# Optimization experiments

Hardware: AMD Instinct MI355X
Metric: run time of the kernel (lower is better)

The kernel has to match this reference:

```python
import jax, jax.numpy as jnp
import numpy as np

B, S, D = 4, 512, 128


def setup_inputs() -> dict:
    key = jax.random.key(0)
    ks = jax.random.split(key, 9)
    scale = 1.0 / np.sqrt(D)
    return {
        "inputs": jax.random.normal(ks[0], (B, S, D), dtype=jnp.float32),
        "encoder_outputs": jax.random.normal(ks[1], (B, S, D), dtype=jnp.float32),
        "mask": jax.random.randint(ks[2], (B, S), 0, 2, dtype=jnp.int32),
        "W1": jax.random.uniform(ks[3], (D, D), jnp.float32, -scale, scale),
        "b1": jax.random.uniform(ks[4], (D,), jnp.float32, -scale, scale),
        "W2": jax.random.uniform(ks[5], (D, D), jnp.float32, -scale, scale),
        "b2": jax.random.uniform(ks[6], (D,), jnp.float32, -scale, scale),
        "v_w": jax.random.uniform(ks[7], (D,), jnp.float32, -scale, scale),
        "v_b": jax.random.uniform(ks[8], (1,), jnp.float32, -scale, scale),
    }


def reference(inputs, encoder_outputs, mask, W1, b1, W2, b2, v_w, v_b):
    # key_out: W1(encoder_outputs)  [B, S_k, D]
    key_out = jnp.einsum("bkd,de->bke", encoder_outputs, W1) + b1
    # query_out: W2(inputs)        [B, S_q, D]
    query_out = jnp.einsum("bqd,de->bqe", inputs, W2) + b2
    # additive attention, all query positions at once: [B, S_q, S_k, D]
    t = jnp.tanh(key_out[:, None, :, :] + query_out[:, :, None, :])
    ui = jnp.einsum("bqkd,d->bqk", t, v_w) + v_b[0]
    # mask out padded key positions for every query position
    valid = mask.astype(bool)[:, None, :]  # [B, 1, S_k]
    logits = jnp.where(valid, ui, -jnp.inf)
    preds = jnp.argmax(logits, axis=-1)
    return (logits, preds)
```

## Files before the change

kernel.cpp:

```cpp
#include <hip/hip_runtime.h>
#include <math.h>

#define NB 4
#define NS 512
#define ND 128

static constexpr float K2LE = 2.885390081777927f;

__device__ inline float fast_exp2(float x){
#if __has_builtin(__builtin_amdgcn_exp2f)
  return __builtin_amdgcn_exp2f(x);
#else
  float r; asm("v_exp_f32 %0, %1" : "=v"(r) : "v"(x)); return r;
#endif
}
__device__ inline float fast_rcp(float x){
#if __has_builtin(__builtin_amdgcn_rcpf)
  return __builtin_amdgcn_rcpf(x);
#else
  float r; asm("v_rcp_f32 %0, %1" : "=v"(r) : "v"(x)); return r;
#endif
}

__global__ __launch_bounds__(256) void proj_kernel(
    const float* __restrict__ inputs, const float* __restrict__ enc,
    const float* __restrict__ W1, const float* __restrict__ b1,
    const float* __restrict__ W2, const float* __restrict__ b2,
    const float* __restrict__ vw, const float* __restrict__ vb,
    float* __restrict__ EKT, float* __restrict__ RQ, float* __restrict__ WQ,
    float* __restrict__ Csum){
  const int ROWS = 16;
  int blk = blockIdx.x;
  int t = threadIdx.x;

  if (blk == 256){
    if (t < 64){
      float v = vw[t] + vw[t + 64];
      #pragma unroll
      for (int off = 32; off; off >>= 1) v += __shfl_down(v, off);
      if (t == 0) Csum[0] = v + vb[0];
    }
    return;
  }

  bool is_key = (blk < 128);
  int rbase = (is_key ? blk : blk - 128) * ROWS;
  const float* X    = is_key ? enc : inputs;
  const float* W    = is_key ? W1  : W2;
  const float* bias = is_key ? b1  : b2;

  __shared__ float rows[ROWS][ND];
  {
    const float4* src = (const float4*)(X + (size_t)rbase*ND);
    float4* dst = (float4*)(&rows[0][0]);
    dst[t]       = src[t];
    dst[t + 256] = src[t + 256];
  }
  __syncthreads();

  int rg = t >> 5;
  int ec = (t & 31) * 4;
  float4 b4 = *(const float4*)(bias + ec);
  float4 acc0 = b4, acc1 = b4;
  const float* r0 = rows[rg];
  const float* r1 = rows[rg + 8];
  const float* wp = W + ec;
  #pragma unroll 4
  for (int d = 0; d < ND; ++d){
    float4 w4 = *(const float4*)(wp + (size_t)d*ND);
    float a = r0[d], c = r1[d];
    acc0.x = fmaf(a, w4.x, acc0.x);  acc1.x = fmaf(c, w4.x, acc1.x);
    acc0.y = fmaf(a, w4.y, acc0.y);  acc1.y = fmaf(c, w4.y, acc1.y);
    acc0.z = fmaf(a, w4.z, acc0.z);  acc1.z = fmaf(c, w4.z, acc1.z);
    acc0.w = fmaf(a, w4.w, acc0.w);  acc1.w = fmaf(c, w4.w, acc1.w);
  }

  if (is_key){
    int b    = rbase >> 9;
    int sloc = rbase & (NS - 1);
    __syncthreads();
    rows[rg][ec+0]   = fast_exp2(K2LE*acc0.x);
    rows[rg][ec+1]   = fast_exp2(K2LE*acc0.y);
    rows[rg][ec+2]   = fast_exp2(K2LE*acc0.z);
    rows[rg][ec+3]   = fast_exp2(K2LE*acc0.w);
    rows[rg+8][ec+0] = fast_exp2(K2LE*acc1.x);
    rows[rg+8][ec+1] = fast_exp2(K2LE*acc1.y);
    rows[rg+8][ec+2] = fast_exp2(K2LE*acc1.z);
    rows[rg+8][ec+3] = fast_exp2(K2LE*acc1.w);
    __syncthreads();
    #pragma unroll
    for (int rep = 0; rep < 2; ++rep){
      int idx = t + rep*256;
      int e  = idx >> 2;
      int sc = (idx & 3) * 4;
      float4 v = { rows[sc+0][e], rows[sc+1][e], rows[sc+2][e], rows[sc+3][e] };
      *(float4*)(EKT + ((size_t)b*ND + e)*NS + sloc + sc) = v;
    }
  } else {
    int row0 = rbase + rg, row1 = row0 + 8;
    float4 vw4 = *(const float4*)(vw + ec);
    float4 r4a, r4b, w4a, w4b;
    r4a.x = fast_exp2(-K2LE*acc0.x);  r4b.x = fast_exp2(-K2LE*acc1.x);
    r4a.y = fast_exp2(-K2LE*acc0.y);  r4b.y = fast_exp2(-K2LE*acc1.y);
    r4a.z = fast_exp2(-K2LE*acc0.z);  r4b.z = fast_exp2(-K2LE*acc1.z);
    r4a.w = fast_exp2(-K2LE*acc0.w);  r4b.w = fast_exp2(-K2LE*acc1.w);
    w4a.x = -2.0f*vw4.x*r4a.x;  w4b.x = -2.0f*vw4.x*r4b.x;
    w4a.y = -2.0f*vw4.y*r4a.y;  w4b.y = -2.0f*vw4.y*r4b.y;
    w4a.z = -2.0f*vw4.z*r4a.z;  w4b.z = -2.0f*vw4.z*r4b.z;
    w4a.w = -2.0f*vw4.w*r4a.w;  w4b.w = -2.0f*vw4.w*r4b.w;
    *(float4*)(RQ + (size_t)row0*ND + ec) = r4a;
    *(float4*)(WQ + (size_t)row0*ND + ec) = w4a;
    *(float4*)(RQ + (size_t)row1*ND + ec) = r4b;
    *(float4*)(WQ + (size_t)row1*ND + ec) = w4b;
  }
}

__global__ __launch_bounds__(512) void score_kernel(
    const float* __restrict__ EKT, const float* __restrict__ RQg,
    const float* __restrict__ WQg, const int* __restrict__ mask,
    const float* __restrict__ Csum, float* __restrict__ out){
  int blk = blockIdx.x;
  int b  = blk >> 7;
  int q0 = (blk & 127) * 4;
  int t  = threadIdx.x;

  __shared__ float RQs[4*ND];
  __shared__ float WQs[4*ND];
  {
    size_t base = (size_t)(b*NS + q0) * ND;
    RQs[t] = RQg[base + t];
    WQs[t] = WQg[base + t];
  }
  __syncthreads();

  const float* ekp = EKT + (size_t)b*ND*NS + t;
  float acc[4] = {0.f, 0.f, 0.f, 0.f};

  #pragma unroll 2
  for (int d = 0; d < ND; d += 4){
    float4 rq4[4], wq4[4];
    #pragma unroll
    for (int qi = 0; qi < 4; ++qi){
      rq4[qi] = *(const float4*)&RQs[qi*ND + d];
      wq4[qi] = *(const float4*)&WQs[qi*ND + d];
    }
    float ek0 = ekp[(size_t)(d+0)*NS];
    float ek1 = ekp[(size_t)(d+1)*NS];
    float ek2 = ekp[(size_t)(d+2)*NS];
    float ek3 = ekp[(size_t)(d+3)*NS];
    #pragma unroll
    for (int qi = 0; qi < 4; ++qi){
      const float* rqf = (const float*)&rq4[qi];
      const float* wqf = (const float*)&wq4[qi];
      acc[qi] = fmaf(wqf[0], fast_rcp(ek0 + rqf[0]), acc[qi]);
      acc[qi] = fmaf(wqf[1], fast_rcp(ek1 + rqf[1]), acc[qi]);
      acc[qi] = fmaf(wqf[2], fast_rcp(ek2 + rqf[2]), acc[qi]);
      acc[qi] = fmaf(wqf[3], fast_rcp(ek3 + rqf[3]), acc[qi]);
    }
  }

  float C = Csum[0];
  int m = mask[b*NS + t];
  const float NINF = -3.0e38f;
  float u[4];
  #pragma unroll
  for (int qi = 0; qi < 4; ++qi) u[qi] = m ? (C + acc[qi]) : NINF;

  float* logits = out;
  float* preds  = out + (size_t)NB*NS*NS;
  {
    size_t base = (size_t)(b*NS + q0) * NS + t;
    logits[base]        = u[0];
    logits[base +   NS] = u[1];
    logits[base + 2*NS] = u[2];
    logits[base + 3*NS] = u[3];
  }

  int lane = t & 63, wv = t >> 6;
  __shared__ float red_v[8][4];
  __shared__ int   red_i[8][4];
  #pragma unroll
  for (int qi = 0; qi < 4; ++qi){
    float v = u[qi]; int idx = t;
    #pragma unroll
    for (int off = 32; off; off >>= 1){
      float ov = __shfl_down(v, off);
      int   oi = __shfl_down(idx, off);
      if (ov > v || (ov == v && oi < idx)){ v = ov; idx = oi; }
    }
    if (lane == 0){ red_v[wv][qi] = v; red_i[wv][qi] = idx; }
  }
  __syncthreads();
  if (t < 4){
    float v = red_v[0][t]; int idx = red_i[0][t];
    #pragma unroll
    for (int w = 1; w < 8; ++w){
      float ov = red_v[w][t]; int oi = red_i[w][t];
      if (ov > v || (ov == v && oi < idx)){ v = ov; idx = oi; }
    }
    preds[b*NS + q0 + t] = (float)idx;
  }
}

extern "C" void kernel_launch(void* const* d_in, const int* in_sizes, int n_in,
                              void* d_out, int out_size, void* d_ws, size_t ws_size,
                              hipStream_t stream){
  const float* inputs = (const float*)d_in[0];
  const float* enc    = (const float*)d_in[1];
  const int*   mask   = (const int*)d_in[2];
  const float* W1     = (const float*)d_in[3];
  const float* b1     = (const float*)d_in[4];
  const float* W2     = (const float*)d_in[5];
  const float* b2     = (const float*)d_in[6];
  const float* vw     = (const float*)d_in[7];
  const float* vb     = (const float*)d_in[8];
  float* out = (float*)d_out;

  float* ws  = (float*)d_ws;
  float* EKT = ws;
  float* RQ  = ws + 262144;
  float* WQ  = ws + 524288;
  float* Cs  = ws + 786432;

  proj_kernel <<<dim3(257), dim3(256), 0, stream>>>(inputs, enc, W1, b1, W2, b2,
                                                    vw, vb, EKT, RQ, WQ, Cs);
  score_kernel<<<dim3(512), dim3(512), 0, stream>>>(EKT, RQ, WQ, mask, Cs, out);
}
```

Baseline: 105.1 us.

## Interleave key projection as float4 over d and read query rows directly

The transposed key tensor is stored in a layout where each float4 holds four consecutive feature values for one key position. The score kernel can then fetch four d-values with one vectorized load instead of four strided scalar loads. The score kernel also drops its shared-memory staging of the query rows and barrier, reading the uniform query rows straight from global memory. The projection kernel now processes 8 rows per block with double the blocks, which gives more parallelism but less reuse of each W load.

```diff
diff --git a/kernel.cpp b/kernel.cpp
--- a/kernel.cpp
+++ b/kernel.cpp
@@ -4,6 +4,7 @@
 #define NB 4
 #define NS 512
 #define ND 128
+#define ND4 32
 
 static constexpr float K2LE = 2.885390081777927f;
 
@@ -27,13 +28,12 @@
     const float* __restrict__ W1, const float* __restrict__ b1,
     const float* __restrict__ W2, const float* __restrict__ b2,
     const float* __restrict__ vw, const float* __restrict__ vb,
-    float* __restrict__ EKT, float* __restrict__ RQ, float* __restrict__ WQ,
+    float* __restrict__ EKT4, float* __restrict__ RQ, float* __restrict__ WQ,
     float* __restrict__ Csum){
-  const int ROWS = 16;
   int blk = blockIdx.x;
   int t = threadIdx.x;
 
-  if (blk == 256){
+  if (blk == 512){
     if (t < 64){
       float v = vw[t] + vw[t + 64];
       #pragma unroll
@@ -43,80 +43,71 @@
     return;
   }
 
-  bool is_key = (blk < 128);
-  int rbase = (is_key ? blk : blk - 128) * ROWS;
+  bool is_key = (blk < 256);
+  int rbase = (is_key ? blk : blk - 256) * 8;
   const float* X    = is_key ? enc : inputs;
   const float* W    = is_key ? W1  : W2;
   const float* bias = is_key ? b1  : b2;
 
-  __shared__ float rows[ROWS][ND];
+  __shared__ float rows[8][132];
   {
-    const float4* src = (const float4*)(X + (size_t)rbase*ND);
-    float4* dst = (float4*)(&rows[0][0]);
-    dst[t]       = src[t];
-    dst[t + 256] = src[t + 256];
+    int r = t >> 5, c4 = (t & 31) * 4;
+    *(float4*)&rows[r][c4] = *(const float4*)(X + (size_t)(rbase + r)*ND + c4);
   }
   __syncthreads();
 
   int rg = t >> 5;
   int ec = (t & 31) * 4;
-  float4 b4 = *(const float4*)(bias + ec);
-  float4 acc0 = b4, acc1 = b4;
-  const float* r0 = rows[rg];
-  const float* r1 = rows[rg + 8];
-  const float* wp = W + ec;
-  #pragma unroll 4
-  for (int d = 0; d < ND; ++d){
-    float4 w4 = *(const float4*)(wp + (size_t)d*ND);
-    float a = r0[d], c = r1[d];
-    acc0.x = fmaf(a, w4.x, acc0.x);  acc1.x = fmaf(c, w4.x, acc1.x);
-    acc0.y = fmaf(a, w4.y, acc0.y);  acc1.y = fmaf(c, w4.y, acc1.y);
-    acc0.z = fmaf(a, w4.z, acc0.z);  acc1.z = fmaf(c, w4.z, acc1.z);
-    acc0.w = fmaf(a, w4.w, acc0.w);  acc1.w = fmaf(c, w4.w, acc1.w);
+  float4 acc = *(const float4*)(bias + ec);
+  #pragma unroll 2
+  for (int d4 = 0; d4 < ND4; ++d4){
+    float4 x4 = *(const float4*)&rows[rg][4*d4];
+    const float* wp = W + (size_t)(4*d4)*ND + ec;
+    float4 w0 = *(const float4*)(wp);
+    float4 w1 = *(const float4*)(wp + ND);
+    float4 w2 = *(const float4*)(wp + 2*ND);
+    float4 w3 = *(const float4*)(wp + 3*ND);
+    acc.x = fmaf(x4.x, w0.x, acc.x); acc.y = fmaf(x4.x, w0.y, acc.y);
+    acc.z = fmaf(x4.x, w0.z, acc.z); acc.w = fmaf(x4.x, w0.w, acc.w);
+    acc.x = fmaf(x4.y, w1.x, acc.x); acc.y = fmaf(x4.y, w1.y, acc.y);
+    acc.z = fmaf(x4.y, w1.z, acc.z); acc.w = fmaf(x4.y, w1.w, acc.w);
+    acc.x = fmaf(x4.z, w2.x, acc.x); acc.y = fmaf(x4.z, w2.y, acc.y);
+    acc.z = fmaf(x4.z, w2.z, acc.z); acc.w = fmaf(x4.z, w2.w, acc.w);
+    acc.x = fmaf(x4.w, w3.x, acc.x); acc.y = fmaf(x4.w, w3.y, acc.y);
+    acc.z = fmaf(x4.w, w3.z, acc.z); acc.w = fmaf(x4.w, w3.w, acc.w);
   }
 
   if (is_key){
     int b    = rbase >> 9;
     int sloc = rbase & (NS - 1);
     __syncthreads();
-    rows[rg][ec+0]   = fast_exp2(K2LE*acc0.x);
-    rows[rg][ec+1]   = fast_exp2(K2LE*acc0.y);
-    rows[rg][ec+2]   = fast_exp2(K2LE*acc0.z);
-    rows[rg][ec+3]   = fast_exp2(K2LE*acc0.w);
-    rows[rg+8][ec+0] = fast_exp2(K2LE*acc1.x);
-    rows[rg+8][ec+1] = fast_exp2(K2LE*acc1.y);
-    rows[rg+8][ec+2] = fast_exp2(K2LE*acc1.z);
-    rows[rg+8][ec+3] = fast_exp2(K2LE*acc1.w);
+    rows[rg][ec+0] = fast_exp2(K2LE*acc.x);
+    rows[rg][ec+1] = fast_exp2(K2LE*acc.y);
+    rows[rg][ec+2] = fast_exp2(K2LE*acc.z);
+    rows[rg][ec+3] = fast_exp2(K2LE*acc.w);
     __syncthreads();
-    #pragma unroll
-    for (int rep = 0; rep < 2; ++rep){
-      int idx = t + rep*256;
-      int e  = idx >> 2;
-      int sc = (idx & 3) * 4;
-      float4 v = { rows[sc+0][e], rows[sc+1][e], rows[sc+2][e], rows[sc+3][e] };
-      *(float4*)(EKT + ((size_t)b*ND + e)*NS + sloc + sc) = v;
-    }
+    int d4 = t >> 3, sl = t & 7;
+    float4 v = *(const float4*)&rows[sl][4*d4];
+    ((float4*)EKT4)[((size_t)(b*ND4 + d4))*NS + sloc + sl] = v;
   } else {
-    int row0 = rbase + rg, row1 = row0 + 8;
+    int row = rbase + rg;
     float4 vw4 = *(const float4*)(vw + ec);
-    float4 r4a, r4b, w4a, w4b;
-    r4a.x = fast_exp2(-K2LE*acc0.x);  r4b.x = fast_exp2(-K2LE*acc1.x);
-    r4a.y = fast_exp2(-K2LE*acc0.y);  r4b.y = fast_exp2(-K2LE*acc1.y);
-    r4a.z = fast_exp2(-K2LE*acc0.z);  r4b.z = fast_exp2(-K2LE*acc1.z);
-    r4a.w = fast_exp2(-K2LE*acc0.w);  r4b.w = fast_exp2(-K2LE*acc1.w);
-    w4a.x = -2.0f*vw4.x*r4a.x;  w4b.x = -2.0f*vw4.x*r4b.x;
-    w4a.y = -2.0f*vw4.y*r4a.y;  w4b.y = -2.0f*vw4.y*r4b.y;
-    w4a.z = -2.0f*vw4.z*r4a.z;  w4b.z = -2.0f*vw4.z*r4b.z;
-    w4a.w = -2.0f*vw4.w*r4a.w;  w4b.w = -2.0f*vw4.w*r4b.w;
-    *(float4*)(RQ + (size_t)row0*ND + ec) = r4a;
-    *(float4*)(WQ + (size_t)row0*ND + ec) = w4a;
-    *(float4*)(RQ + (size_t)row1*ND + ec) = r4b;
-    *(float4*)(WQ + (size_t)row1*ND + ec) = w4b;
+    float4 r4, w4;
+    r4.x = fast_exp2(-K2LE*acc.x);
+    r4.y = fast_exp2(-K2LE*acc.y);
+    r4.z = fast_exp2(-K2LE*acc.z);
+    r4.w = fast_exp2(-K2LE*acc.w);
+    w4.x = -2.0f*vw4.x*r4.x;
+    w4.y = -2.0f*vw4.y*r4.y;
+    w4.z = -2.0f*vw4.z*r4.z;
+    w4.w = -2.0f*vw4.w*r4.w;
+    *(float4*)(RQ + (size_t)row*ND + ec) = r4;
+    *(float4*)(WQ + (size_t)row*ND + ec) = w4;
   }
 }
 
 __global__ __launch_bounds__(512) void score_kernel(
-    const float* __restrict__ EKT, const float* __restrict__ RQg,
+    const float* __restrict__ EKT4, const float* __restrict__ RQg,
     const float* __restrict__ WQg, const int* __restrict__ mask,
     const float* __restrict__ Csum, float* __restrict__ out){
   int blk = blockIdx.x;
@@ -124,47 +115,50 @@
   int q0 = (blk & 127) * 4;
   int t  = threadIdx.x;
 
-  __shared__ float RQs[4*ND];
-  __shared__ float WQs[4*ND];
-  {
-    size_t base = (size_t)(b*NS + q0) * ND;
-    RQs[t] = RQg[base + t];
-    WQs[t] = WQg[base + t];
-  }
-  __syncthreads();
-
-  const float* ekp = EKT + (size_t)b*ND*NS + t;
-  float acc[4] = {0.f, 0.f, 0.f, 0.f};
-
-  #pragma unroll 2
-  for (int d = 0; d < ND; d += 4){
-    float4 rq4[4], wq4[4];
-    #pragma unroll
-    for (int qi = 0; qi < 4; ++qi){
-      rq4[qi] = *(const float4*)&RQs[qi*ND + d];
-      wq4[qi] = *(const float4*)&WQs[qi*ND + d];
-    }
-    float ek0 = ekp[(size_t)(d+0)*NS];
-    float ek1 = ekp[(size_t)(d+1)*NS];
-    float ek2 = ekp[(size_t)(d+2)*NS];
-    float ek3 = ekp[(size_t)(d+3)*NS];
-    #pragma unroll
-    for (int qi = 0; qi < 4; ++qi){
-      const float* rqf = (const float*)&rq4[qi];
-      const float* wqf = (const float*)&wq4[qi];
-      acc[qi] = fmaf(wqf[0], fast_rcp(ek0 + rqf[0]), acc[qi]);
-      acc[qi] = fmaf(wqf[1], fast_rcp(ek1 + rqf[1]), acc[qi]);
-      acc[qi] = fmaf(wqf[2], fast_rcp(ek2 + rqf[2]), acc[qi]);
-      acc[qi] = fmaf(wqf[3], fast_rcp(ek3 + rqf[3]), acc[qi]);
-    }
-  }
+  const float4* ek4 = (const float4*)EKT4 + (size_t)(b*ND4)*NS + t;
+  const float* rq = RQg + (size_t)(b*NS + q0)*ND;
+  const float* wq = WQg + (size_t)(b*NS + q0)*ND;
 
   float C = Csum[0];
   int m = mask[b*NS + t];
+
+  float a0=0.f, a1=0.f, a2=0.f, a3=0.f;
+  #pragma unroll 2
+  for (int d4 = 0; d4 < ND4; ++d4){
+    float4 ek = ek4[(size_t)d4*NS];
+    int d = 4*d4;
+    float4 r0 = *(const float4*)(rq + d);
+    float4 r1 = *(const float4*)(rq + ND + d);
+    float4 r2 = *(const float4*)(rq + 2*ND + d);
+    float4 r3 = *(const float4*)(rq + 3*ND + d);
+    float4 w0 = *(const float4*)(wq + d);
+    float4 w1 = *(const float4*)(wq + ND + d);
+    float4 w2 = *(const float4*)(wq + 2*ND + d);
+    float4 w3 = *(const float4*)(wq + 3*ND + d);
+    a0 = fmaf(w0.x, fast_rcp(ek.x + r0.x), a0);
+    a0 = fmaf(w0.y, fast_rcp(ek.y + r0.y), a0);
+    a0 = fmaf(w0.z, fast_rcp(ek.z + r0.z), a0);
+    a0 = fmaf(w0.w, fast_rcp(ek.w + r0.w), a0);
+    a1 = fmaf(w1.x, fast_rcp(ek.x + r1.x), a1);
+    a1 = fmaf(w1.y, fast_rcp(ek.y + r1.y), a1);
+    a1 = fmaf(w1.z, fast_rcp(ek.z + r1.z), a1);
+    a1 = fmaf(w1.w, fast_rcp(ek.w + r1.w), a1);
+    a2 = fmaf(w2.x, fast_rcp(ek.x + r2.x), a2);
+    a2 = fmaf(w2.y, fast_rcp(ek.y + r2.y), a2);
+    a2 = fmaf(w2.z, fast_rcp(ek.z + r2.z), a2);
+    a2 = fmaf(w2.w, fast_rcp(ek.w + r2.w), a2);
+    a3 = fmaf(w3.x, fast_rcp(ek.x + r3.x), a3);
+    a3 = fmaf(w3.y, fast_rcp(ek.y + r3.y), a3);
+    a3 = fmaf(w3.z, fast_rcp(ek.z + r3.z), a3);
+    a3 = fmaf(w3.w, fast_rcp(ek.w + r3.w), a3);
+  }
+
   const float NINF = -3.0e38f;
   float u[4];
-  #pragma unroll
-  for (int qi = 0; qi < 4; ++qi) u[qi] = m ? (C + acc[qi]) : NINF;
+  u[0] = m ? (C + a0) : NINF;
+  u[1] = m ? (C + a1) : NINF;
+  u[2] = m ? (C + a2) : NINF;
+  u[3] = m ? (C + a3) : NINF;
 
   float* logits = out;
   float* preds  = out + (size_t)NB*NS*NS;
@@ -216,13 +210,13 @@
   const float* vb     = (const float*)d_in[8];
   float* out = (float*)d_out;
 
-  float* ws  = (float*)d_ws;
-  float* EKT = ws;
-  float* RQ  = ws + 262144;
-  float* WQ  = ws + 524288;
-  float* Cs  = ws + 786432;
-
-  proj_kernel <<<dim3(257), dim3(256), 0, stream>>>(inputs, enc, W1, b1, W2, b2,
-                                                    vw, vb, EKT, RQ, WQ, Cs);
-  score_kernel<<<dim3(512), dim3(512), 0, stream>>>(EKT, RQ, WQ, mask, Cs, out);
-}
+  float* ws   = (float*)d_ws;
+  float* EKT4 = ws;
+  float* RQ   = ws + 262144;
+  float* WQ   = ws + 524288;
+  float* Cs   = ws + 786432;
+
+  proj_kernel <<<dim3(513), dim3(256), 0, stream>>>(inputs, enc, W1, b1, W2, b2,
+                                                    vw, vb, EKT4, RQ, WQ, Cs);
+  score_kernel<<<dim3(512), dim3(512), 0, stream>>>(EKT4, RQ, WQ, mask, Cs, out);
+}
```

After: 99.72 us. 1.05x faster.
